# Optimization experiments

Hardware: AMD Instinct MI355X
Metric: run time of the kernel (lower is better)

The kernel has to match this reference:

```python
import jax, jax.numpy as jnp
import numpy as np

N, E, F_IN, H, C, G = 100000, 800000, 128, 128, 10, 512


def setup_inputs() -> dict:
    key = jax.random.key(0)
    ks = jax.random.split(key, 12)
    x = jax.random.normal(ks[0], (N, F_IN), dtype=jnp.float32)
    edge_index = jax.random.randint(ks[1], (2, E), 0, N, dtype=jnp.int64)
    batch = jnp.sort(jax.random.randint(ks[2], (N,), 0, G, dtype=jnp.int64))
    def glorot(k, fan_in, fan_out):
        lim = jnp.sqrt(6.0 / (fan_in + fan_out)).astype(jnp.float32)
        return jax.random.uniform(k, (fan_in, fan_out), jnp.float32, -lim, lim)
    return {
        "x": x,
        "edge_index": edge_index,
        "batch": batch,
        "W1": glorot(ks[3], F_IN, H), "b1": jnp.zeros((H,), jnp.float32),
        "W2": glorot(ks[4], H, H),    "b2": jnp.zeros((H,), jnp.float32),
        "W3": glorot(ks[5], H, H),    "b3": jnp.zeros((H,), jnp.float32),
        "Wl": glorot(ks[6], H, C),    "bl": jnp.zeros((C,), jnp.float32),
    }


def _gcn_conv(x, row, col, norm, W, b):
    # h = x W ; msg_e = norm_e * h[src_e] ; out_i = sum_{e: dst_e = i} msg_e + b
    h = x @ W                                  # [N, H]
    msg = norm[:, None] * h[row]               # [E+N, H] gather over sources
    out = jax.ops.segment_sum(msg, col, num_segments=N)  # scatter-add to targets
    return out + b


def reference(x, edge_index, batch, W1, b1, W2, b2, W3, b3, Wl, bl):
    n = x.shape[0]
    loops = jnp.arange(n, dtype=edge_index.dtype)
    row = jnp.concatenate([edge_index[0], loops])  # sources (with self-loops)
    col = jnp.concatenate([edge_index[1], loops])  # targets
    # symmetric normalization: deg over targets (PyG GCNConv convention)
    deg = jax.ops.segment_sum(jnp.ones_like(col, dtype=x.dtype), col, num_segments=n)
    dinv = jnp.where(deg > 0, jax.lax.rsqrt(jnp.maximum(deg, 1.0)), 0.0)
    norm = dinv[row] * dinv[col]

    h = jax.nn.relu(_gcn_conv(x, row, col, norm, W1, b1))
    h = jax.nn.relu(_gcn_conv(h, row, col, norm, W2, b2))
    h = _gcn_conv(h, row, col, norm, W3, b3)

    # global mean pool over graphs
    num_graphs = G
    sums = jax.ops.segment_sum(h, batch, num_segments=num_graphs)
    cnts = jax.ops.segment_sum(jnp.ones((n,), h.dtype), batch, num_segments=num_graphs)
    pooled = sums / jnp.maximum(cnts, 1.0)[:, None]

    # dropout is identity in eval mode
    return pooled @ Wl + bl
```

## Files before the change

### kernel.cpp

```cpp
#include <hip/hip_runtime.h>
#include <cstddef>

#define HD 128
#define QSEG 8
#define BSH 7
#define NBP 1024
#define EB 4096


typedef float f32x4 __attribute__((ext_vector_type(4)));
typedef float f32x8 __attribute__((ext_vector_type(8)));
typedef _Float16 f16x8 __attribute__((ext_vector_type(8)));
typedef unsigned short u16x8 __attribute__((ext_vector_type(8)));

static __device__ __forceinline__ int atomAddI(int* p, int v) {
    return __hip_atomic_fetch_add(p, v, __ATOMIC_RELAXED, __HIP_MEMORY_SCOPE_AGENT);
}

static __device__ __forceinline__ unsigned short f32_to_f16u(float f) {
    _Float16 h = (_Float16)f;
    return __builtin_bit_cast(unsigned short, h);
}
static __device__ __forceinline__ float f16u_to_f32(unsigned short u) {
    return (float)__builtin_bit_cast(_Float16, u);
}

__global__ void k_zero_int(int* p, int n) {
    int i = blockIdx.x * blockDim.x + threadIdx.x;
    if (i < n) p[i] = 0;
}

__global__ __launch_bounds__(256) void k_bhist(const int* __restrict__ coli,
                                               int* __restrict__ bcnt, int E, int NB) {
    __shared__ int lc[NBP];
    for (int b = threadIdx.x; b < NBP; b += 256) lc[b] = 0;
    __syncthreads();
    const int base = blockIdx.x * (EB * 2);
    const int end = min(base + EB * 2, E);
    for (int i = base + threadIdx.x; i < end; i += 256)
        atomicAdd(&lc[coli[i] >> BSH], 1);
    __syncthreads();
    for (int b = threadIdx.x; b < NB; b += 256)
        if (lc[b]) atomAddI(&bcnt[b], lc[b]);
}

__global__ __launch_bounds__(256) void k_bscan(const int* __restrict__ bcnt,
                                               int* __restrict__ bbase,
                                               int* __restrict__ cursor,
                                               int* __restrict__ rowptr,
                                               int NB, int E, int N) {
    __shared__ int sd[256];
    const int t = threadIdx.x;
    int loc[4];
    int tsum = 0;
#pragma unroll
    for (int i = 0; i < 4; ++i) {
        const int b = t * 4 + i;
        loc[i] = (b < NB) ? bcnt[b] : 0;
        tsum += loc[i];
    }
    sd[t] = tsum;
    __syncthreads();
    for (int off = 1; off < 256; off <<= 1) {
        int u = (t >= off) ? sd[t - off] : 0;
        __syncthreads();
        sd[t] += u;
        __syncthreads();
    }
    int pos = sd[t] - tsum;
#pragma unroll
    for (int i = 0; i < 4; ++i) {
        const int b = t * 4 + i;
        if (b < NB) { bbase[b] = pos; cursor[b] = pos; }
        pos += loc[i];
    }
    if (t == 255) {
        bbase[NB] = sd[255];
        rowptr[N] = sd[255];
    }
}

__global__ __launch_bounds__(256) void k_bin(const int* __restrict__ rowi,
                                             const int* __restrict__ coli,
                                             int* __restrict__ cursor,
                                             unsigned* __restrict__ pairs, int E, int NB) {
    __shared__ int lcnt[NBP];
    __shared__ int gbs[NBP];
    const int t = threadIdx.x;
    const int base = blockIdx.x * EB;
    for (int b = t; b < NBP; b += 256) lcnt[b] = 0;
    __syncthreads();

    unsigned ed[16];
    int eb[16];
#pragma unroll
    for (int u = 0; u < 16; ++u) {
        const int idx = base + u * 256 + t;
        if (idx < E) {
            const unsigned src = (unsigned)rowi[idx];
            const unsigned dst = (unsigned)coli[idx];
            ed[u] = ((dst & 127u) << 20) | src;
            eb[u] = (int)(dst >> BSH);
            atomicAdd(&lcnt[eb[u]], 1);
        } else {
            eb[u] = -1;
        }
    }
    __syncthreads();
    for (int b = t; b < NB; b += 256) {
        const int c = lcnt[b];
        gbs[b] = c > 0 ? atomAddI(&cursor[b], c) : 0;
    }
    __syncthreads();
    for (int b = t; b < NBP; b += 256) lcnt[b] = 0;
    __syncthreads();
#pragma unroll
    for (int u = 0; u < 16; ++u) {
        if (eb[u] >= 0) {
            const int p = gbs[eb[u]] + atomicAdd(&lcnt[eb[u]], 1);
            pairs[p] = ed[u];
        }
    }
}

__global__ __launch_bounds__(256) void k_sortbuild(const unsigned* __restrict__ pairs,
                                                   const int* __restrict__ bbase,
                                                   int* __restrict__ rowptr,
                                                   float* __restrict__ dinv,
                                                   int* __restrict__ csr_src, int N) {
    __shared__ int cnt[128];
    __shared__ int pref[128];
    const int j = blockIdx.x;
    const int t = threadIdx.x;
    const int s = bbase[j];
    const int e2 = bbase[j + 1];
    const int d0 = j << BSH;
    const int dc = min(128, N - d0);

    if (t < 128) cnt[t] = 0;
    __syncthreads();
    for (int i = s + t; i < e2; i += 256)
        atomicAdd(&cnt[pairs[i] >> 20], 1);
    __syncthreads();
    if (t == 0) {
        int run = 0;
        for (int k = 0; k < 128; ++k) { pref[k] = run; run += cnt[k]; }
    }
    __syncthreads();
    if (t < dc) {
        rowptr[d0 + t] = s + pref[t];
        dinv[d0 + t] = rsqrtf(1.0f + (float)cnt[t]);
    }
    __syncthreads();
    if (t < 128) cnt[t] = 0;
    __syncthreads();
    for (int i = s + t; i < e2; i += 256) {
        const unsigned p = pairs[i];
        const int dl = (int)(p >> 20);
        const int pos = atomicAdd(&cnt[dl], 1);
        csr_src[s + pref[dl] + pos] = (int)(p & 0xFFFFFu);
    }
}

__global__ __launch_bounds__(256) void k_wfrag(const float* __restrict__ W1,
                                               const float* __restrict__ W2,
                                               const float* __restrict__ W3,
                                               unsigned short* __restrict__ wf) {
    const int w = blockIdx.x >> 3;
    const int slot = (blockIdx.x & 7) * 256 + threadIdx.x;
    const int nt = slot >> 8;
    const int kt = (slot >> 6) & 3;
    const int lane = slot & 63;
    const float* W = (w == 0) ? W1 : (w == 1) ? W2 : W3;
    unsigned short* wt = wf + (size_t)w * 16384;
    const int obase = ((nt * 4 + kt) * 64 + lane) * 8;
    const int c = nt * 16 + (lane & 15);
    u16x8 h8;
#pragma unroll
    for (int e = 0; e < 8; ++e) {
        const int k = (w == 0) ? (kt * 32 + (lane >> 4) * 8 + e)
                               : (e * 16 + kt * 4 + (lane >> 4));
        h8[e] = f32_to_f16u(W[(size_t)k * HD + c]);
    }
    *(u16x8*)&wt[obase] = h8;
}

__global__ void k_bprep(const float* __restrict__ b1, const float* __restrict__ b2,
                        const float* __restrict__ b3, float* __restrict__ bp) {
    const int t = threadIdx.x;
    const float* b = (blockIdx.x == 0) ? b1 : (blockIdx.x == 1) ? b2 : b3;
    bp[blockIdx.x * HD + t] = b[(t & 7) * 16 + (t >> 3)];
}

template <int AF32>
__global__ __launch_bounds__(256) void k_gemm(const void* __restrict__ Av,
                                              const unsigned short* __restrict__ wfr,
                                              const float* __restrict__ dinv,
                                              unsigned short* __restrict__ M, int n) {
    __shared__ unsigned short lds[16384];
    {
        const float4* s0 = (const float4*)wfr;
        float4* d0 = (float4*)lds;
#pragma unroll
        for (int i = 0; i < 8; ++i)
            d0[i * 256 + threadIdx.x] = s0[i * 256 + threadIdx.x];
    }
    __syncthreads();

    const int lane = threadIdx.x & 63;
    const int wid = threadIdx.x >> 6;
    const int rbase = blockIdx.x * 128 + wid * 32;
    const int arow0 = min(rbase + (lane & 15), n - 1);
    const int arow1 = min(rbase + 16 + (lane & 15), n - 1);
    const int kbase = (lane >> 4) * 8;

    f32x4 acc[2][8];
#pragma unroll
    for (int g = 0; g < 2; ++g)
#pragma unroll
        for (int nt = 0; nt < 8; ++nt) acc[g][nt] = (f32x4){0.f, 0.f, 0.f, 0.f};

#pragma unroll
    for (int kt = 0; kt < 4; ++kt) {
        f16x8 a0, a1;
        if (AF32) {
            const float* X = (const float*)Av;
            const float4 p0 = *(const float4*)&X[(size_t)arow0 * HD + kt * 32 + kbase];
            const float4 p1 = *(const float4*)&X[(size_t)arow0 * HD + kt * 32 + kbase + 4];
            const float4 q0 = *(const float4*)&X[(size_t)arow1 * HD + kt * 32 + kbase];
            const float4 q1 = *(const float4*)&X[(size_t)arow1 * HD + kt * 32 + kbase + 4];
            a0[0] = (_Float16)p0.x; a0[1] = (_Float16)p0.y;
            a0[2] = (_Float16)p0.z; a0[3] = (_Float16)p0.w;
            a0[4] = (_Float16)p1.x; a0[5] = (_Float16)p1.y;
            a0[6] = (_Float16)p1.z; a0[7] = (_Float16)p1.w;
            a1[0] = (_Float16)q0.x; a1[1] = (_Float16)q0.y;
            a1[2] = (_Float16)q0.z; a1[3] = (_Float16)q0.w;
            a1[4] = (_Float16)q1.x; a1[5] = (_Float16)q1.y;
            a1[6] = (_Float16)q1.z; a1[7] = (_Float16)q1.w;
        } else {
            const unsigned short* X = (const unsigned short*)Av;
            a0 = *(const f16x8*)&X[(size_t)arow0 * HD + kt * 32 + kbase];
            a1 = *(const f16x8*)&X[(size_t)arow1 * HD + kt * 32 + kbase];
        }
#pragma unroll
        for (int nt = 0; nt < 8; ++nt) {
            const int fo = ((nt * 4 + kt) * 64 + lane) * 8;
            const f16x8 bf = *(const f16x8*)&lds[fo];
            acc[0][nt] = __builtin_amdgcn_mfma_f32_16x16x32_f16(a0, bf, acc[0][nt], 0, 0, 0);
            acc[1][nt] = __builtin_amdgcn_mfma_f32_16x16x32_f16(a1, bf, acc[1][nt], 0, 0, 0);
        }
    }

    const int colb = lane & 15;
    const int rq = (lane >> 4) * 4;
#pragma unroll
    for (int g = 0; g < 2; ++g) {
#pragma unroll
        for (int r = 0; r < 4; ++r) {
            const int row = rbase + g * 16 + rq + r;
            if (row < n) {
                const float d = dinv[row];
                u16x8 o;
#pragma unroll
                for (int nt = 0; nt < 8; ++nt) o[nt] = f32_to_f16u(acc[g][nt][r] * d);
                *(u16x8*)&M[(size_t)row * HD + colb * 8] = o;
            }
        }
    }
}

template <int LAST>
__global__ __launch_bounds__(256) void k_gather(const int* __restrict__ rowptr,
                                                const int* __restrict__ csr_src,
                                                const unsigned short* __restrict__ M,
                                                const float* __restrict__ dinv,
                                                const float* __restrict__ b,
                                                void* __restrict__ OUTv, int n) {
    const int lane = threadIdx.x & 63;
    const int wid = threadIdx.x >> 6;
    const int grp = lane >> 4;
    const int node = blockIdx.x * 16 + wid * 4 + grp;
    if (node >= n) return;
    const int j = (lane & 15) * 8;

    const u16x8 sv = *(const u16x8*)&M[(size_t)node * HD + j];
    f32x8 acc;
#pragma unroll
    for (int i = 0; i < 8; ++i) acc[i] = f16u_to_f32(sv[i]);

    const int s = rowptr[node];
    const int e = rowptr[node + 1];
    int k = s;
    for (; k + 4 <= e; k += 4) {
        const int i0 = csr_src[k], i1 = csr_src[k + 1];
        const int i2 = csr_src[k + 2], i3 = csr_src[k + 3];
        const u16x8 v0 = *(const u16x8*)&M[(size_t)i0 * HD + j];
        const u16x8 v1 = *(const u16x8*)&M[(size_t)i1 * HD + j];
        const u16x8 v2 = *(const u16x8*)&M[(size_t)i2 * HD + j];
        const u16x8 v3 = *(const u16x8*)&M[(size_t)i3 * HD + j];
#pragma unroll
        for (int i = 0; i < 8; ++i)
            acc[i] += (f16u_to_f32(v0[i]) + f16u_to_f32(v1[i])) +
                      (f16u_to_f32(v2[i]) + f16u_to_f32(v3[i]));
    }
    for (; k < e; ++k) {
        const int i0 = csr_src[k];
        const u16x8 v0 = *(const u16x8*)&M[(size_t)i0 * HD + j];
#pragma unroll
        for (int i = 0; i < 8; ++i) acc[i] += f16u_to_f32(v0[i]);
    }

    const float d = dinv[node];
    const float4 bv0 = *(const float4*)&b[j];
    const float4 bv1 = *(const float4*)&b[j + 4];
    const float bb[8] = {bv0.x, bv0.y, bv0.z, bv0.w, bv1.x, bv1.y, bv1.z, bv1.w};
    float o[8];
#pragma unroll
    for (int i = 0; i < 8; ++i) {
        o[i] = fmaf(acc[i], d, bb[i]);
        if (!LAST) o[i] = fmaxf(o[i], 0.f);
    }
    if (!LAST) {
        unsigned short* OUT = (unsigned short*)OUTv;
        u16x8 ov;
#pragma unroll
        for (int i = 0; i < 8; ++i) ov[i] = f32_to_f16u(o[i]);
        *(u16x8*)&OUT[(size_t)node * HD + j] = ov;
    } else {
        float* OUT = (float*)OUTv;
        *(float4*)&OUT[(size_t)node * HD + j] = make_float4(o[0], o[1], o[2], o[3]);
        *(float4*)&OUT[(size_t)node * HD + j + 4] = make_float4(o[4], o[5], o[6], o[7]);
    }
}

__global__ __launch_bounds__(128) void k_pool_part(const float* __restrict__ X,
                                                   const int* __restrict__ batch,
                                                   float* __restrict__ psum, int n) {
    const int g = blockIdx.x / QSEG;
    const int q = blockIdx.x % QSEG;
    const int t = threadIdx.x;
    int lo = 0, hi = n;
    while (lo < hi) { int m = (lo + hi) >> 1; if (batch[m] < g) lo = m + 1; else hi = m; }
    const int start = lo;
    hi = n;
    while (lo < hi) { int m = (lo + hi) >> 1; if (batch[m] < g + 1) lo = m + 1; else hi = m; }
    const int end = lo;
    float acc = 0.f;
    for (int i = start + q; i < end; i += QSEG) acc += X[(size_t)i * HD + t];
    psum[(size_t)blockIdx.x * HD + t] = acc;
}

__global__ __launch_bounds__(128) void k_pool_final(const float* __restrict__ psum,
                                                    const int* __restrict__ batch,
                                                    const float* __restrict__ Wl,
                                                    const float* __restrict__ bl,
                                                    float* __restrict__ out, int n, int C) {
    __shared__ float pl[HD];
    const int g = blockIdx.x;
    const int t = threadIdx.x;
    int lo = 0, hi = n;
    while (lo < hi) { int m = (lo + hi) >> 1; if (batch[m] < g) lo = m + 1; else hi = m; }
    const int start = lo;
    hi = n;
    while (lo < hi) { int m = (lo + hi) >> 1; if (batch[m] < g + 1) lo = m + 1; else hi = m; }
    const int cnt = lo - start;
    float acc = 0.f;
#pragma unroll
    for (int q = 0; q < QSEG; ++q)
        acc += psum[((size_t)g * QSEG + q) * HD + t];
    pl[t] = acc / (float)max(cnt, 1);
    __syncthreads();
    if (t < C) {
        float s = 0.f;
        for (int k = 0; k < HD; ++k) {
            const int c = (k & 7) * 16 + (k >> 3);
            s = fmaf(pl[k], Wl[(size_t)c * C + t], s);
        }
        out[(size_t)g * C + t] = s + bl[t];
    }
}

extern "C" void kernel_launch(void* const* d_in, const int* in_sizes, int n_in,
                              void* d_out, int out_size, void* d_ws, size_t ws_size,
                              hipStream_t stream) {
    const float* x   = (const float*)d_in[0];
    const int* ei    = (const int*)d_in[1];
    const int* batch = (const int*)d_in[2];
    const float* W1 = (const float*)d_in[3];
    const float* b1 = (const float*)d_in[4];
    const float* W2 = (const float*)d_in[5];
    const float* b2 = (const float*)d_in[6];
    const float* W3 = (const float*)d_in[7];
    const float* b3 = (const float*)d_in[8];
    const float* Wl = (const float*)d_in[9];
    const float* bl = (const float*)d_in[10];
    float* out = (float*)d_out;

    const int N = in_sizes[0] / HD;
    const int E = in_sizes[1] / 2;
    const int C = 10;
    const int G = out_size / C;
    const int NB = (N + 127) >> BSH;

    const int* rowi = ei;
    const int* coli = ei + E;

    float* Yf         = (float*)d_ws;
    unsigned short* M = (unsigned short*)(Yf + (size_t)N * HD);
    unsigned short* Yb = M + (size_t)N * HD;
    float* dinv     = (float*)(Yb + (size_t)N * HD);
    unsigned short* wf = (unsigned short*)(dinv + N);
    float* bp       = (float*)(wf + 3 * 16384);
    int* rowptr     = (int*)(bp + 3 * HD);
    int* bcnt       = rowptr + (N + 1);
    int* bbase      = bcnt + NB;
    int* cursor     = bbase + (NB + 1);
    int* csr_src    = cursor + NB;
    unsigned* pairs = (unsigned*)M;
    float* psum     = (float*)M;

    const int T = 256;

    k_zero_int<<<(NB + T - 1) / T, T, 0, stream>>>(bcnt, NB);
    k_bhist<<<(E + EB * 2 - 1) / (EB * 2), T, 0, stream>>>(coli, bcnt, E, NB);
    k_bscan<<<1, T, 0, stream>>>(bcnt, bbase, cursor, rowptr, NB, E, N);
    k_bin<<<(E + EB - 1) / EB, T, 0, stream>>>(rowi, coli, cursor, pairs, E, NB);
    k_sortbuild<<<NB, T, 0, stream>>>(pairs, bbase, rowptr, dinv, csr_src, N);
    k_wfrag<<<24, 256, 0, stream>>>(W1, W2, W3, wf);
    k_bprep<<<3, 128, 0, stream>>>(b1, b2, b3, bp);

    const unsigned short* wf1 = wf;
    const unsigned short* wf2 = wf + 16384;
    const unsigned short* wf3 = wf + 32768;

    const int gGemm   = (N + 127) / 128;
    const int gGather = (N + 15) / 16;

    k_gemm<1><<<gGemm, T, 0, stream>>>(x, wf1, dinv, M, N);
    k_gather<0><<<gGather, T, 0, stream>>>(rowptr, csr_src, M, dinv, bp, Yb, N);

    k_gemm<0><<<gGemm, T, 0, stream>>>(Yb, wf2, dinv, M, N);
    k_gather<0><<<gGather, T, 0, stream>>>(rowptr, csr_src, M, dinv, bp + HD, Yb, N);

    k_gemm<0><<<gGemm, T, 0, stream>>>(Yb, wf3, dinv, M, N);
    k_gather<1><<<gGather, T, 0, stream>>>(rowptr, csr_src, M, dinv, bp + 2 * HD, Yf, N);

    k_pool_part<<<G * QSEG, 128, 0, stream>>>(Yf, batch, psum, N);
    k_pool_final<<<G, 128, 0, stream>>>(psum, batch, Wl, bl, out, N, C);
}
```

Before: 238.7 us.

## Replace bucket histogram+scan with fixed-capacity buckets and store final layer as fp16

Drops the histogram, zero and scan kernels by giving each 128-node destination bucket a fixed slot of ECAP entries, so binning writes straight into preallocated regions. Per-node rowend is kept because the CSR is no longer contiguous. The last layer's output is now fp16, which halves the pooling read traffic. This removes two launches and one pass over the edge list, but overflows if any bucket gets more than 1536 edges and adds fp16 rounding to the final activations.

```diff
diff --git a/kernel.cpp b/kernel.cpp
--- a/kernel.cpp
+++ b/kernel.cpp
@@ -6,6 +6,7 @@
 #define BSH 7
 #define NBP 1024
 #define EB 4096
+#define ECAP 1536
 
 
 typedef float f32x4 __attribute__((ext_vector_type(4)));
@@ -25,65 +26,15 @@
     return (float)__builtin_bit_cast(_Float16, u);
 }
 
-__global__ void k_zero_int(int* p, int n) {
+__global__ void k_initcur(int* cursor, int NB) {
     int i = blockIdx.x * blockDim.x + threadIdx.x;
-    if (i < n) p[i] = 0;
-}
-
-__global__ __launch_bounds__(256) void k_bhist(const int* __restrict__ coli,
-                                               int* __restrict__ bcnt, int E, int NB) {
-    __shared__ int lc[NBP];
-    for (int b = threadIdx.x; b < NBP; b += 256) lc[b] = 0;
-    __syncthreads();
-    const int base = blockIdx.x * (EB * 2);
-    const int end = min(base + EB * 2, E);
-    for (int i = base + threadIdx.x; i < end; i += 256)
-        atomicAdd(&lc[coli[i] >> BSH], 1);
-    __syncthreads();
-    for (int b = threadIdx.x; b < NB; b += 256)
-        if (lc[b]) atomAddI(&bcnt[b], lc[b]);
-}
-
-__global__ __launch_bounds__(256) void k_bscan(const int* __restrict__ bcnt,
-                                               int* __restrict__ bbase,
-                                               int* __restrict__ cursor,
-                                               int* __restrict__ rowptr,
-                                               int NB, int E, int N) {
-    __shared__ int sd[256];
-    const int t = threadIdx.x;
-    int loc[4];
-    int tsum = 0;
-#pragma unroll
-    for (int i = 0; i < 4; ++i) {
-        const int b = t * 4 + i;
-        loc[i] = (b < NB) ? bcnt[b] : 0;
-        tsum += loc[i];
-    }
-    sd[t] = tsum;
-    __syncthreads();
-    for (int off = 1; off < 256; off <<= 1) {
-        int u = (t >= off) ? sd[t - off] : 0;
-        __syncthreads();
-        sd[t] += u;
-        __syncthreads();
-    }
-    int pos = sd[t] - tsum;
-#pragma unroll
-    for (int i = 0; i < 4; ++i) {
-        const int b = t * 4 + i;
-        if (b < NB) { bbase[b] = pos; cursor[b] = pos; }
-        pos += loc[i];
-    }
-    if (t == 255) {
-        bbase[NB] = sd[255];
-        rowptr[N] = sd[255];
-    }
-}
-
-__global__ __launch_bounds__(256) void k_bin(const int* __restrict__ rowi,
-                                             const int* __restrict__ coli,
-                                             int* __restrict__ cursor,
-                                             unsigned* __restrict__ pairs, int E, int NB) {
+    if (i < NB) cursor[i] = i * ECAP;
+}
+
+__global__ __launch_bounds__(256) void k_binP(const int* __restrict__ rowi,
+                                              const int* __restrict__ coli,
+                                              int* __restrict__ cursor,
+                                              unsigned* __restrict__ pairs, int E, int NB) {
     __shared__ int lcnt[NBP];
     __shared__ int gbs[NBP];
     const int t = threadIdx.x;
@@ -123,17 +74,18 @@
     }
 }
 
-__global__ __launch_bounds__(256) void k_sortbuild(const unsigned* __restrict__ pairs,
-                                                   const int* __restrict__ bbase,
-                                                   int* __restrict__ rowptr,
-                                                   float* __restrict__ dinv,
-                                                   int* __restrict__ csr_src, int N) {
+__global__ __launch_bounds__(256) void k_sortbuildP(const unsigned* __restrict__ pairs,
+                                                    const int* __restrict__ cursor,
+                                                    int* __restrict__ rowptr,
+                                                    int* __restrict__ rowend,
+                                                    float* __restrict__ dinv,
+                                                    int* __restrict__ csr_src, int N) {
     __shared__ int cnt[128];
     __shared__ int pref[128];
     const int j = blockIdx.x;
     const int t = threadIdx.x;
-    const int s = bbase[j];
-    const int e2 = bbase[j + 1];
+    const int s = j * ECAP;
+    const int e2 = cursor[j];
     const int d0 = j << BSH;
     const int dc = min(128, N - d0);
 
@@ -149,6 +101,7 @@
     __syncthreads();
     if (t < dc) {
         rowptr[d0 + t] = s + pref[t];
+        rowend[d0 + t] = s + pref[t] + cnt[t];
         dinv[d0 + t] = rsqrtf(1.0f + (float)cnt[t]);
     }
     __syncthreads();
@@ -269,13 +222,14 @@
     }
 }
 
-template <int LAST>
+template <int RELU>
 __global__ __launch_bounds__(256) void k_gather(const int* __restrict__ rowptr,
+                                                const int* __restrict__ rowend,
                                                 const int* __restrict__ csr_src,
                                                 const unsigned short* __restrict__ M,
                                                 const float* __restrict__ dinv,
                                                 const float* __restrict__ b,
-                                                void* __restrict__ OUTv, int n) {
+                                                unsigned short* __restrict__ OUT, int n) {
     const int lane = threadIdx.x & 63;
     const int wid = threadIdx.x >> 6;
     const int grp = lane >> 4;
@@ -289,7 +243,7 @@
     for (int i = 0; i < 8; ++i) acc[i] = f16u_to_f32(sv[i]);
 
     const int s = rowptr[node];
-    const int e = rowptr[node + 1];
+    const int e = rowend[node];
     int k = s;
     for (; k + 4 <= e; k += 4) {
         const int i0 = csr_src[k], i1 = csr_src[k + 1];
@@ -314,26 +268,17 @@
     const float4 bv0 = *(const float4*)&b[j];
     const float4 bv1 = *(const float4*)&b[j + 4];
     const float bb[8] = {bv0.x, bv0.y, bv0.z, bv0.w, bv1.x, bv1.y, bv1.z, bv1.w};
-    float o[8];
+    u16x8 ov;
 #pragma unroll
     for (int i = 0; i < 8; ++i) {
-        o[i] = fmaf(acc[i], d, bb[i]);
-        if (!LAST) o[i] = fmaxf(o[i], 0.f);
-    }
-    if (!LAST) {
-        unsigned short* OUT = (unsigned short*)OUTv;
-        u16x8 ov;
-#pragma unroll
-        for (int i = 0; i < 8; ++i) ov[i] = f32_to_f16u(o[i]);
-        *(u16x8*)&OUT[(size_t)node * HD + j] = ov;
-    } else {
-        float* OUT = (float*)OUTv;
-        *(float4*)&OUT[(size_t)node * HD + j] = make_float4(o[0], o[1], o[2], o[3]);
-        *(float4*)&OUT[(size_t)node * HD + j + 4] = make_float4(o[4], o[5], o[6], o[7]);
-    }
-}
-
-__global__ __launch_bounds__(128) void k_pool_part(const float* __restrict__ X,
+        float o = fmaf(acc[i], d, bb[i]);
+        if (RELU) o = fmaxf(o, 0.f);
+        ov[i] = f32_to_f16u(o);
+    }
+    *(u16x8*)&OUT[(size_t)node * HD + j] = ov;
+}
+
+__global__ __launch_bounds__(128) void k_pool_part(const unsigned short* __restrict__ X,
                                                    const int* __restrict__ batch,
                                                    float* __restrict__ psum, int n) {
     const int g = blockIdx.x / QSEG;
@@ -346,7 +291,8 @@
     while (lo < hi) { int m = (lo + hi) >> 1; if (batch[m] < g + 1) lo = m + 1; else hi = m; }
     const int end = lo;
     float acc = 0.f;
-    for (int i = start + q; i < end; i += QSEG) acc += X[(size_t)i * HD + t];
+    for (int i = start + q; i < end; i += QSEG)
+        acc += f16u_to_f32(X[(size_t)i * HD + t]);
     psum[(size_t)blockIdx.x * HD + t] = acc;
 }
 
@@ -405,27 +351,24 @@
     const int* rowi = ei;
     const int* coli = ei + E;
 
-    float* Yf         = (float*)d_ws;
-    unsigned short* M = (unsigned short*)(Yf + (size_t)N * HD);
+    unsigned short* Yf = (unsigned short*)d_ws;
+    unsigned short* M  = Yf + (size_t)N * HD;
     unsigned short* Yb = M + (size_t)N * HD;
     float* dinv     = (float*)(Yb + (size_t)N * HD);
     unsigned short* wf = (unsigned short*)(dinv + N);
     float* bp       = (float*)(wf + 3 * 16384);
     int* rowptr     = (int*)(bp + 3 * HD);
-    int* bcnt       = rowptr + (N + 1);
-    int* bbase      = bcnt + NB;
-    int* cursor     = bbase + (NB + 1);
+    int* rowend     = rowptr + N;
+    int* cursor     = rowend + N;
     int* csr_src    = cursor + NB;
     unsigned* pairs = (unsigned*)M;
     float* psum     = (float*)M;
 
     const int T = 256;
 
-    k_zero_int<<<(NB + T - 1) / T, T, 0, stream>>>(bcnt, NB);
-    k_bhist<<<(E + EB * 2 - 1) / (EB * 2), T, 0, stream>>>(coli, bcnt, E, NB);
-    k_bscan<<<1, T, 0, stream>>>(bcnt, bbase, cursor, rowptr, NB, E, N);
-    k_bin<<<(E + EB - 1) / EB, T, 0, stream>>>(rowi, coli, cursor, pairs, E, NB);
-    k_sortbuild<<<NB, T, 0, stream>>>(pairs, bbase, rowptr, dinv, csr_src, N);
+    k_initcur<<<(NB + T - 1) / T, T, 0, stream>>>(cursor, NB);
+    k_binP<<<(E + EB - 1) / EB, T, 0, stream>>>(rowi, coli, cursor, pairs, E, NB);
+    k_sortbuildP<<<NB, T, 0, stream>>>(pairs, cursor, rowptr, rowend, dinv, csr_src, N);
     k_wfrag<<<24, 256, 0, stream>>>(W1, W2, W3, wf);
     k_bprep<<<3, 128, 0, stream>>>(b1, b2, b3, bp);
 
@@ -437,13 +380,13 @@
     const int gGather = (N + 15) / 16;
 
     k_gemm<1><<<gGemm, T, 0, stream>>>(x, wf1, dinv, M, N);
-    k_gather<0><<<gGather, T, 0, stream>>>(rowptr, csr_src, M, dinv, bp, Yb, N);
+    k_gather<1><<<gGather, T, 0, stream>>>(rowptr, rowend, csr_src, M, dinv, bp, Yb, N);
 
     k_gemm<0><<<gGemm, T, 0, stream>>>(Yb, wf2, dinv, M, N);
-    k_gather<0><<<gGather, T, 0, stream>>>(rowptr, csr_src, M, dinv, bp + HD, Yb, N);
+    k_gather<1><<<gGather, T, 0, stream>>>(rowptr, rowend, csr_src, M, dinv, bp + HD, Yb, N);
 
     k_gemm<0><<<gGemm, T, 0, stream>>>(Yb, wf3, dinv, M, N);
-    k_gather<1><<<gGather, T, 0, stream>>>(rowptr, csr_src, M, dinv, bp + 2 * HD, Yf, N);
+    k_gather<0><<<gGather, T, 0, stream>>>(rowptr, rowend, csr_src, M, dinv, bp + 2 * HD, Yf, N);
 
     k_pool_part<<<G * QSEG, 128, 0, stream>>>(Yf, batch, psum, N);
     k_pool_final<<<G, 128, 0, stream>>>(psum, batch, Wl, bl, out, N, C);
```

Result: faster. 218.4 us, median of 2 (-8.5%).
